# Kernel tuning notes

Hardware: AMD Instinct MI355X
Metric: run time of the kernel (lower is better)

## Reference

```python
import jax, jax.numpy as jnp
import numpy as np

N = 4096
C = 8192
D = 64
MARGIN = 0.1
ALPHA = 32.0


def setup_inputs() -> dict:
    key = jax.random.key(0)
    k1, k2, k3, k4 = jax.random.split(key, 4)
    embeddings = jax.random.normal(k1, (N, D), dtype=jnp.float32)
    labels = jax.random.randint(k2, (N,), 0, C)
    # kaiming_normal_(mode='fan_out') on a (C, D) tensor -> std = sqrt(2/C)
    mean_proxies = jax.random.normal(k3, (C, D), dtype=jnp.float32) * np.sqrt(2.0 / C)
    log_variance_proxies = jax.random.normal(k4, (C, D), dtype=jnp.float32) * np.sqrt(2.0 / C)
    return {
        "embeddings": embeddings,
        "labels": labels,
        "mean_proxies": mean_proxies,
        "log_variance_proxies": log_variance_proxies,
    }


def _mls_scores(e, mu, logvar):
    """score[i,j] = -0.5 * sum_d[(e_id - mu_jd)^2 * exp(-logvar_jd) + logvar_jd].
    Expanded into GEMMs to avoid materializing the (N, C, D) broadcast tensor."""
    inv_var = jnp.exp(-logvar)                                  # (C, D)
    e2_term = (e * e) @ inv_var.T                               # (N, C)
    cross = e @ (mu * inv_var).T                                # (N, C)
    const = jnp.sum(mu * mu * inv_var + logvar, axis=1)         # (C,)
    return -0.5 * (e2_term - 2.0 * cross + const[None, :])      # (N, C)


def reference(embeddings, labels, mean_proxies, log_variance_proxies):
    score_mat = _mls_scores(embeddings, mean_proxies, log_variance_proxies)  # (N, C)
    pos_mask = jax.nn.one_hot(labels, C, dtype=score_mat.dtype)              # (N, C)

    pos_e = -ALPHA * (score_mat - MARGIN)
    neg_e = ALPHA * (score_mat + MARGIN)
    m = jnp.max(pos_e)  # NOTE: original code uses max(pos_exp) for BOTH terms
    pos_exp = jnp.exp(pos_e - m)
    neg_exp = jnp.exp(neg_e - m)

    counts = jnp.sum(pos_mask, axis=0)                   # (C,)
    num_valid = jnp.sum(counts != 0).astype(score_mat.dtype)

    pos_sim_sum = jnp.sum(jnp.where(pos_mask == 1, pos_exp, 0.0), axis=0)  # (C,)
    neg_sim_sum = jnp.sum(jnp.where(pos_mask == 0, neg_exp, 0.0), axis=0)  # (C,)

    pos_term = jnp.sum(jnp.log1p(pos_sim_sum) + m) / num_valid
    neg_term = jnp.sum(jnp.log1p(neg_sim_sum) + m) / C
    return pos_term + neg_term
```

## Files before the change

kernel.cpp:

```cpp
#include <hip/hip_runtime.h>
#include <hip/hip_bf16.h>
#include <math.h>


#define N_EMB 4096
#define C_CLS 8192
#define D_DIM 64
#define K_DIM 128

typedef __attribute__((ext_vector_type(8))) __bf16 bf16x8;
typedef __attribute__((ext_vector_type(16))) float f32x16;
typedef __attribute__((ext_vector_type(4))) int i32x4;

__device__ __forceinline__ void async_ld16(void* lds, const void* g) {
  __builtin_amdgcn_global_load_lds(
      (__attribute__((address_space(1))) void*)g,
      (__attribute__((address_space(3))) void*)lds, 16, 0, 0);
}

__global__ void k_prep(const float* __restrict__ emb,
                       const float* __restrict__ mp,
                       const float* __restrict__ lvp,
                       __bf16* __restrict__ wsA,
                       __bf16* __restrict__ wsB,
                       float* __restrict__ constv) {
  int wave = (int)((blockIdx.x * blockDim.x + threadIdx.x) >> 6);
  int lane = threadIdx.x & 63;
  if (wave < N_EMB) {
    float e = emb[wave * D_DIM + lane];
    wsA[wave * K_DIM + lane]         = (__bf16)(e * e);
    wsA[wave * K_DIM + D_DIM + lane] = (__bf16)e;
  } else {
    int j = wave - N_EMB;
    float mu = mp[j * D_DIM + lane];
    float lv = lvp[j * D_DIM + lane];
    float iv = __expf(-lv);
    wsB[j * K_DIM + lane]         = (__bf16)iv;
    wsB[j * K_DIM + D_DIM + lane] = (__bf16)(-2.0f * mu * iv);
    float t = fmaf(mu * mu, iv, lv);
    #pragma unroll
    for (int s = 32; s >= 1; s >>= 1) t += __shfl_xor(t, s);
    if (lane == 0) constv[j] = t;
  }
}

__global__ __launch_bounds__(256, 2) void k_main(
    const __bf16* __restrict__ wsA, const __bf16* __restrict__ wsB,
    const float* __restrict__ constv, const int* __restrict__ labels,
    float* __restrict__ wsM, float* __restrict__ wsP, float* __restrict__ wsN) {
  __shared__ __align__(16) char As[32768];
  __shared__ __align__(16) char Bs[32768];

  const int tid = threadIdx.x;
  const int rb = blockIdx.x & 31;
  const int cb = blockIdx.x >> 5;

  const char* Ag = (const char*)(wsA + (size_t)rb * 128 * K_DIM);
  const char* Bg = (const char*)(wsB + (size_t)cb * 128 * K_DIM);
  #pragma unroll
  for (int it = 0; it < 8; ++it) {
    int L = it * 256 + tid;
    int r = L >> 4, cs = L & 15;
    int goff = r * 256 + ((cs ^ (r & 15)) << 4);
    async_ld16(As + L * 16, Ag + goff);
  }
  #pragma unroll
  for (int it = 0; it < 8; ++it) {
    int L = it * 256 + tid;
    int r = L >> 4, cs = L & 15;
    int goff = r * 256 + ((cs ^ (r & 15)) << 4);
    async_ld16(Bs + L * 16, Bg + goff);
  }
  __syncthreads();

  const int wv = tid >> 6, lane = tid & 63;
  const int wr = wv >> 1, wc = wv & 1;
  const int l31 = lane & 31, kg = lane >> 5;
  const int l15 = lane & 15;

  f32x16 acc[2][2];
  #pragma unroll
  for (int mi = 0; mi < 2; ++mi)
    #pragma unroll
    for (int ni = 0; ni < 2; ++ni)
      #pragma unroll
      for (int r = 0; r < 16; ++r) acc[mi][ni][r] = 0.f;

  #pragma unroll
  for (int kk = 0; kk < 8; ++kk) {
    const int c = kk * 2 + kg;
    const int cofs = (c ^ l15) << 4;
    bf16x8 af[2], bfr[2];
    #pragma unroll
    for (int mi = 0; mi < 2; ++mi)
      af[mi] = *(const bf16x8*)(As + (wr * 64 + mi * 32 + l31) * 256 + cofs);
    #pragma unroll
    for (int ni = 0; ni < 2; ++ni)
      bfr[ni] = *(const bf16x8*)(Bs + (wc * 64 + ni * 32 + l31) * 256 + cofs);
    #pragma unroll
    for (int mi = 0; mi < 2; ++mi)
      #pragma unroll
      for (int ni = 0; ni < 2; ++ni)
        acc[mi][ni] = __builtin_amdgcn_mfma_f32_32x32x16_bf16(
            af[mi], bfr[ni], acc[mi][ni], 0, 0, 0);
  }

  __syncthreads();
  float* colred = (float*)As;
  int* labels_s = (int*)(As + 3072);
  float* pc_s   = (float*)(As + 3584);
  if (tid < 128) {
    labels_s[tid] = labels[rb * 128 + tid];
    pc_s[tid] = fmaf(16.0f, constv[cb * 128 + tid], 3.2f);
  }
  __syncthreads();

  i32x4 labv[2][4];
  #pragma unroll
  for (int mi = 0; mi < 2; ++mi)
    #pragma unroll
    for (int g = 0; g < 4; ++g)
      labv[mi][g] = *(const i32x4*)&labels_s[wr * 64 + mi * 32 + 4 * kg + 8 * g];

  #pragma unroll
  for (int ni = 0; ni < 2; ++ni) {
    const int col_local = wc * 64 + ni * 32 + l31;
    const int gcol = cb * 128 + col_local;
    const float pcv = pc_s[col_local];
    float lmax = -1e30f;
    #pragma unroll
    for (int mi = 0; mi < 2; ++mi)
      #pragma unroll
      for (int r = 0; r < 16; ++r)
        lmax = fmaxf(lmax, fmaf(16.0f, acc[mi][ni][r], pcv));
    lmax = fmaxf(lmax, __shfl_xor(lmax, 32));
    float ps = 0.f, ns = 0.f;
    #pragma unroll
    for (int mi = 0; mi < 2; ++mi)
      #pragma unroll
      for (int r = 0; r < 16; ++r) {
        float pe = fmaf(16.0f, acc[mi][ni][r], pcv);
        bool match = (labv[mi][r >> 2][r & 3] == gcol);
        float v = match ? pe : (6.4f - pe);
        float ex = __expf(v - lmax);
        ps += match ? ex : 0.f;
        ns += match ? 0.f : ex;
      }
    ps += __shfl_xor(ps, 32);
    ns += __shfl_xor(ns, 32);
    if (kg == 0) {
      float* cr = &colred[(wr * 128 + col_local) * 3];
      cr[0] = lmax; cr[1] = ps; cr[2] = ns;
    }
  }
  __syncthreads();
  if (tid < 128) {
    const float* c0 = &colred[(0 * 128 + tid) * 3];
    const float* c1 = &colred[(1 * 128 + tid) * 3];
    float M = fmaxf(c0[0], c1[0]);
    float s0 = __expf(c0[0] - M), s1 = __expf(c1[0] - M);
    int gcol = cb * 128 + tid;
    wsM[rb * C_CLS + gcol] = M;
    wsP[rb * C_CLS + gcol] = fmaf(c0[1], s0, c1[1] * s1);
    wsN[rb * C_CLS + gcol] = fmaf(c0[2], s0, c1[2] * s1);
  }
}

__global__ __launch_bounds__(256) void k_red1(
    const float* __restrict__ wsM, const float* __restrict__ wsP,
    const float* __restrict__ wsN, float* __restrict__ Mcol,
    float* __restrict__ Pcol, float* __restrict__ Ncol) {
  __shared__ float red[4][64][3];
  const int tid = threadIdx.x;
  const int col = tid & 63, part = tid >> 6;
  const int j = blockIdx.x * 64 + col;

  float m8[8];
  float M = -1e30f;
  #pragma unroll
  for (int r = 0; r < 8; ++r) {
    m8[r] = wsM[(part * 8 + r) * C_CLS + j];
    M = fmaxf(M, m8[r]);
  }
  float ps = 0.f, ns = 0.f;
  #pragma unroll
  for (int r = 0; r < 8; ++r) {
    float s = __expf(m8[r] - M);
    ps = fmaf(wsP[(part * 8 + r) * C_CLS + j], s, ps);
    ns = fmaf(wsN[(part * 8 + r) * C_CLS + j], s, ns);
  }
  red[part][col][0] = M; red[part][col][1] = ps; red[part][col][2] = ns;
  __syncthreads();
  if (part == 0) {
    float M0 = red[0][col][0], M1 = red[1][col][0];
    float M2 = red[2][col][0], M3 = red[3][col][0];
    float Mx = fmaxf(fmaxf(M0, M1), fmaxf(M2, M3));
    float s0 = __expf(M0 - Mx), s1 = __expf(M1 - Mx);
    float s2 = __expf(M2 - Mx), s3 = __expf(M3 - Mx);
    Mcol[j] = Mx;
    Pcol[j] = fmaf(red[0][col][1], s0, fmaf(red[1][col][1], s1,
              fmaf(red[2][col][1], s2, red[3][col][1] * s3)));
    Ncol[j] = fmaf(red[0][col][2], s0, fmaf(red[1][col][2], s1,
              fmaf(red[2][col][2], s2, red[3][col][2] * s3)));
  }
}

__global__ __launch_bounds__(1024) void k_fin(
    const float* __restrict__ Mcol, const float* __restrict__ Pcol,
    const float* __restrict__ Ncol, const int* __restrict__ labels,
    float* __restrict__ out) {
  __shared__ unsigned char flag[C_CLS];
  __shared__ float sA[16], sB[16];
  __shared__ int sI[16];
  const int tid = threadIdx.x;
  const int wv = tid >> 6, lane = tid & 63;
  for (int i = tid; i < C_CLS; i += 1024) flag[i] = 0;
  __syncthreads();
  for (int i = tid; i < N_EMB; i += 1024) flag[labels[i]] = 1;
  __syncthreads();
  int nv = 0;
  float gm = -1e30f;
  #pragma unroll
  for (int k = 0; k < C_CLS / 1024; ++k) {
    int i = k * 1024 + tid;
    nv += flag[i];
    gm = fmaxf(gm, Mcol[i]);
  }
  #pragma unroll
  for (int s = 32; s >= 1; s >>= 1) {
    gm = fmaxf(gm, __shfl_xor(gm, s));
    nv += __shfl_xor(nv, s);
  }
  if (lane == 0) { sA[wv] = gm; sI[wv] = nv; }
  __syncthreads();
  if (tid == 0) {
    float mm = -1e30f; int n = 0;
    #pragma unroll
    for (int k = 0; k < 16; ++k) { mm = fmaxf(mm, sA[k]); n += sI[k]; }
    sA[0] = mm; sI[0] = n;
  }
  __syncthreads();
  const float m = sA[0];
  const int num_valid = sI[0];
  __syncthreads();
  float pt = 0.f, nt = 0.f;
  #pragma unroll
  for (int k = 0; k < C_CLS / 1024; ++k) {
    int i = k * 1024 + tid;
    float s = __expf(Mcol[i] - m);
    pt += log1pf(Pcol[i] * s);
    nt += log1pf(Ncol[i] * s);
  }
  #pragma unroll
  for (int s = 32; s >= 1; s >>= 1) {
    pt += __shfl_xor(pt, s);
    nt += __shfl_xor(nt, s);
  }
  if (lane == 0) { sA[wv] = pt; sB[wv] = nt; }
  __syncthreads();
  if (tid == 0) {
    float sp = 0.f, sn = 0.f;
    #pragma unroll
    for (int k = 0; k < 16; ++k) { sp += sA[k]; sn += sB[k]; }
    out[0] = (sp + (float)C_CLS * m) / (float)num_valid
           + (sn + (float)C_CLS * m) / (float)C_CLS;
  }
}

extern "C" void kernel_launch(void* const* d_in, const int* in_sizes, int n_in,
                              void* d_out, int out_size, void* d_ws, size_t ws_size,
                              hipStream_t stream) {
  const float* emb    = (const float*)d_in[0];
  const int*   labels = (const int*)d_in[1];
  const float* mp     = (const float*)d_in[2];
  const float* lvp    = (const float*)d_in[3];
  float* out = (float*)d_out;

  char* ws = (char*)d_ws;
  __bf16* wsA   = (__bf16*)ws;
  __bf16* wsB   = (__bf16*)(ws + (1u << 20));
  float* constv = (float*)(ws + 3u * (1u << 20));
  float* wsM    = (float*)(ws + 3u * (1u << 20) + (1u << 15));
  float* wsP    = wsM + 32 * C_CLS;
  float* wsN    = wsP + 32 * C_CLS;
  float* Mcol   = wsN + 32 * C_CLS;
  float* Pcol   = Mcol + C_CLS;
  float* Ncol   = Pcol + C_CLS;

  hipLaunchKernelGGL(k_prep, dim3((N_EMB + C_CLS) / 4), dim3(256), 0, stream,
                     emb, mp, lvp, wsA, wsB, constv);
  hipLaunchKernelGGL(k_main, dim3((N_EMB / 128) * (C_CLS / 128)), dim3(256), 0, stream,
                     wsA, wsB, constv, labels, wsM, wsP, wsN);
  hipLaunchKernelGGL(k_red1, dim3(128), dim3(256), 0, stream,
                     wsM, wsP, wsN, Mcol, Pcol, Ncol);
  hipLaunchKernelGGL(k_fin, dim3(1), dim3(1024), 0, stream,
                     Mcol, Pcol, Ncol, labels, out);
}
```

Baseline: 102.1 us.

## Loop row tiles inside persistent blocks with double-buffered A loads and drop red1

k_main now launches 256 blocks of 512 threads. Each block keeps one 128-column B tile resident and loops over eight 128-row A tiles, double-buffering them with async LDS loads. The online softmax-style max/sum state is carried in registers across row tiles, so only 4 row-group partials per column are written instead of 32. The k_red1 kernel is removed and its merge folded into k_fin. The intent is to cut launch count, partial-sum traffic and per-block prologue cost, at the price of only 256 blocks for the whole GPU (about one per CU) and less latency hiding.

```diff
diff --git a/kernel.cpp b/kernel.cpp
--- a/kernel.cpp
+++ b/kernel.cpp
@@ -44,188 +44,178 @@
   }
 }
 
-__global__ __launch_bounds__(256, 2) void k_main(
+__global__ __launch_bounds__(512, 1) void k_main(
     const __bf16* __restrict__ wsA, const __bf16* __restrict__ wsB,
     const float* __restrict__ constv, const int* __restrict__ labels,
     float* __restrict__ wsM, float* __restrict__ wsP, float* __restrict__ wsN) {
-  __shared__ __align__(16) char As[32768];
+  __shared__ __align__(16) char As[2][32768];
   __shared__ __align__(16) char Bs[32768];
 
   const int tid = threadIdx.x;
-  const int rb = blockIdx.x & 31;
-  const int cb = blockIdx.x >> 5;
-
-  const char* Ag = (const char*)(wsA + (size_t)rb * 128 * K_DIM);
-  const char* Bg = (const char*)(wsB + (size_t)cb * 128 * K_DIM);
-  #pragma unroll
-  for (int it = 0; it < 8; ++it) {
-    int L = it * 256 + tid;
-    int r = L >> 4, cs = L & 15;
-    int goff = r * 256 + ((cs ^ (r & 15)) << 4);
-    async_ld16(As + L * 16, Ag + goff);
-  }
-  #pragma unroll
-  for (int it = 0; it < 8; ++it) {
-    int L = it * 256 + tid;
+  const int cb = blockIdx.x & 63;
+  const int rg = blockIdx.x >> 6;
+
+  const char* Abase = (const char*)wsA + (size_t)rg * 1024 * 256;
+  const char* Bg    = (const char*)wsB + (size_t)cb * 128 * 256;
+
+  #pragma unroll
+  for (int it = 0; it < 4; ++it) {
+    int L = it * 512 + tid;
     int r = L >> 4, cs = L & 15;
     int goff = r * 256 + ((cs ^ (r & 15)) << 4);
     async_ld16(Bs + L * 16, Bg + goff);
   }
-  __syncthreads();
+  #pragma unroll
+  for (int it = 0; it < 4; ++it) {
+    int L = it * 512 + tid;
+    int r = L >> 4, cs = L & 15;
+    int goff = r * 256 + ((cs ^ (r & 15)) << 4);
+    async_ld16(As[0] + L * 16, Abase + goff);
+  }
 
   const int wv = tid >> 6, lane = tid & 63;
-  const int wr = wv >> 1, wc = wv & 1;
+  const int wc = wv & 1, wr = wv >> 1;
   const int l31 = lane & 31, kg = lane >> 5;
   const int l15 = lane & 15;
 
-  f32x16 acc[2][2];
-  #pragma unroll
-  for (int mi = 0; mi < 2; ++mi)
+  float pcv[2];
+  #pragma unroll
+  for (int ni = 0; ni < 2; ++ni)
+    pcv[ni] = fmaf(16.0f, constv[cb * 128 + wc * 64 + ni * 32 + l31], 3.2f);
+
+  float rM[2] = {-1e30f, -1e30f}, rP[2] = {0.f, 0.f}, rN[2] = {0.f, 0.f};
+
+  __syncthreads();
+
+  for (int t = 0; t < 8; ++t) {
+    if (t < 7) {
+      const char* Agn = Abase + (size_t)(t + 1) * 32768;
+      #pragma unroll
+      for (int it = 0; it < 4; ++it) {
+        int L = it * 512 + tid;
+        int r = L >> 4, cs = L & 15;
+        int goff = r * 256 + ((cs ^ (r & 15)) << 4);
+        async_ld16(As[(t + 1) & 1] + L * 16, Agn + goff);
+      }
+    }
+    const char* Ac = As[t & 1];
+
+    f32x16 acc[2];
     #pragma unroll
     for (int ni = 0; ni < 2; ++ni)
       #pragma unroll
-      for (int r = 0; r < 16; ++r) acc[mi][ni][r] = 0.f;
-
-  #pragma unroll
-  for (int kk = 0; kk < 8; ++kk) {
-    const int c = kk * 2 + kg;
-    const int cofs = (c ^ l15) << 4;
-    bf16x8 af[2], bfr[2];
-    #pragma unroll
-    for (int mi = 0; mi < 2; ++mi)
-      af[mi] = *(const bf16x8*)(As + (wr * 64 + mi * 32 + l31) * 256 + cofs);
-    #pragma unroll
-    for (int ni = 0; ni < 2; ++ni)
-      bfr[ni] = *(const bf16x8*)(Bs + (wc * 64 + ni * 32 + l31) * 256 + cofs);
-    #pragma unroll
-    for (int mi = 0; mi < 2; ++mi)
-      #pragma unroll
-      for (int ni = 0; ni < 2; ++ni)
-        acc[mi][ni] = __builtin_amdgcn_mfma_f32_32x32x16_bf16(
-            af[mi], bfr[ni], acc[mi][ni], 0, 0, 0);
-  }
-
-  __syncthreads();
-  float* colred = (float*)As;
-  int* labels_s = (int*)(As + 3072);
-  float* pc_s   = (float*)(As + 3584);
-  if (tid < 128) {
-    labels_s[tid] = labels[rb * 128 + tid];
-    pc_s[tid] = fmaf(16.0f, constv[cb * 128 + tid], 3.2f);
-  }
-  __syncthreads();
-
-  i32x4 labv[2][4];
-  #pragma unroll
-  for (int mi = 0; mi < 2; ++mi)
+      for (int r = 0; r < 16; ++r) acc[ni][r] = 0.f;
+
+    #pragma unroll
+    for (int kk = 0; kk < 8; ++kk) {
+      const int c = kk * 2 + kg;
+      const int cofs = (c ^ l15) << 4;
+      bf16x8 af = *(const bf16x8*)(Ac + (wr * 32 + l31) * 256 + cofs);
+      bf16x8 b0 = *(const bf16x8*)(Bs + (wc * 64 + l31) * 256 + cofs);
+      bf16x8 b1 = *(const bf16x8*)(Bs + (wc * 64 + 32 + l31) * 256 + cofs);
+      acc[0] = __builtin_amdgcn_mfma_f32_32x32x16_bf16(af, b0, acc[0], 0, 0, 0);
+      acc[1] = __builtin_amdgcn_mfma_f32_32x32x16_bf16(af, b1, acc[1], 0, 0, 0);
+    }
+
+    const int rowbase = rg * 1024 + t * 128 + wr * 32 + 4 * kg;
+    i32x4 labv[4];
     #pragma unroll
     for (int g = 0; g < 4; ++g)
-      labv[mi][g] = *(const i32x4*)&labels_s[wr * 64 + mi * 32 + 4 * kg + 8 * g];
-
-  #pragma unroll
-  for (int ni = 0; ni < 2; ++ni) {
-    const int col_local = wc * 64 + ni * 32 + l31;
-    const int gcol = cb * 128 + col_local;
-    const float pcv = pc_s[col_local];
-    float lmax = -1e30f;
-    #pragma unroll
-    for (int mi = 0; mi < 2; ++mi)
+      labv[g] = *(const i32x4*)&labels[rowbase + 8 * g];
+
+    #pragma unroll
+    for (int ni = 0; ni < 2; ++ni) {
+      const int gcol = cb * 128 + wc * 64 + ni * 32 + l31;
+      float lmax = -1e30f;
       #pragma unroll
       for (int r = 0; r < 16; ++r)
-        lmax = fmaxf(lmax, fmaf(16.0f, acc[mi][ni][r], pcv));
-    lmax = fmaxf(lmax, __shfl_xor(lmax, 32));
-    float ps = 0.f, ns = 0.f;
-    #pragma unroll
-    for (int mi = 0; mi < 2; ++mi)
+        lmax = fmaxf(lmax, fmaf(16.0f, acc[ni][r], pcv[ni]));
+      lmax = fmaxf(lmax, __shfl_xor(lmax, 32));
+      float ps = 0.f, ns = 0.f;
       #pragma unroll
       for (int r = 0; r < 16; ++r) {
-        float pe = fmaf(16.0f, acc[mi][ni][r], pcv);
-        bool match = (labv[mi][r >> 2][r & 3] == gcol);
+        float pe = fmaf(16.0f, acc[ni][r], pcv[ni]);
+        bool match = (labv[r >> 2][r & 3] == gcol);
         float v = match ? pe : (6.4f - pe);
         float ex = __expf(v - lmax);
         ps += match ? ex : 0.f;
         ns += match ? 0.f : ex;
       }
-    ps += __shfl_xor(ps, 32);
-    ns += __shfl_xor(ns, 32);
-    if (kg == 0) {
-      float* cr = &colred[(wr * 128 + col_local) * 3];
-      cr[0] = lmax; cr[1] = ps; cr[2] = ns;
+      ps += __shfl_xor(ps, 32);
+      ns += __shfl_xor(ns, 32);
+      float nM = fmaxf(rM[ni], lmax);
+      float sO = __expf(rM[ni] - nM), sN = __expf(lmax - nM);
+      rP[ni] = fmaf(rP[ni], sO, ps * sN);
+      rN[ni] = fmaf(rN[ni], sO, ns * sN);
+      rM[ni] = nM;
+    }
+    __syncthreads();
+  }
+
+  float* colred = (float*)As[0];
+  if (kg == 0) {
+    #pragma unroll
+    for (int ni = 0; ni < 2; ++ni) {
+      int cl = wc * 64 + ni * 32 + l31;
+      float* cr = &colred[(wr * 128 + cl) * 3];
+      cr[0] = rM[ni]; cr[1] = rP[ni]; cr[2] = rN[ni];
     }
   }
   __syncthreads();
   if (tid < 128) {
-    const float* c0 = &colred[(0 * 128 + tid) * 3];
-    const float* c1 = &colred[(1 * 128 + tid) * 3];
-    float M = fmaxf(c0[0], c1[0]);
-    float s0 = __expf(c0[0] - M), s1 = __expf(c1[0] - M);
+    float M = -1e30f;
+    #pragma unroll
+    for (int w = 0; w < 4; ++w) M = fmaxf(M, colred[(w * 128 + tid) * 3]);
+    float P = 0.f, Nn = 0.f;
+    #pragma unroll
+    for (int w = 0; w < 4; ++w) {
+      const float* cr = &colred[(w * 128 + tid) * 3];
+      float s = __expf(cr[0] - M);
+      P = fmaf(cr[1], s, P);
+      Nn = fmaf(cr[2], s, Nn);
+    }
     int gcol = cb * 128 + tid;
-    wsM[rb * C_CLS + gcol] = M;
-    wsP[rb * C_CLS + gcol] = fmaf(c0[1], s0, c1[1] * s1);
-    wsN[rb * C_CLS + gcol] = fmaf(c0[2], s0, c1[2] * s1);
-  }
-}
-
-__global__ __launch_bounds__(256) void k_red1(
+    wsM[rg * C_CLS + gcol] = M;
+    wsP[rg * C_CLS + gcol] = P;
+    wsN[rg * C_CLS + gcol] = Nn;
+  }
+}
+
+__global__ __launch_bounds__(1024) void k_fin(
     const float* __restrict__ wsM, const float* __restrict__ wsP,
-    const float* __restrict__ wsN, float* __restrict__ Mcol,
-    float* __restrict__ Pcol, float* __restrict__ Ncol) {
-  __shared__ float red[4][64][3];
-  const int tid = threadIdx.x;
-  const int col = tid & 63, part = tid >> 6;
-  const int j = blockIdx.x * 64 + col;
-
-  float m8[8];
-  float M = -1e30f;
-  #pragma unroll
-  for (int r = 0; r < 8; ++r) {
-    m8[r] = wsM[(part * 8 + r) * C_CLS + j];
-    M = fmaxf(M, m8[r]);
-  }
-  float ps = 0.f, ns = 0.f;
-  #pragma unroll
-  for (int r = 0; r < 8; ++r) {
-    float s = __expf(m8[r] - M);
-    ps = fmaf(wsP[(part * 8 + r) * C_CLS + j], s, ps);
-    ns = fmaf(wsN[(part * 8 + r) * C_CLS + j], s, ns);
-  }
-  red[part][col][0] = M; red[part][col][1] = ps; red[part][col][2] = ns;
-  __syncthreads();
-  if (part == 0) {
-    float M0 = red[0][col][0], M1 = red[1][col][0];
-    float M2 = red[2][col][0], M3 = red[3][col][0];
-    float Mx = fmaxf(fmaxf(M0, M1), fmaxf(M2, M3));
-    float s0 = __expf(M0 - Mx), s1 = __expf(M1 - Mx);
-    float s2 = __expf(M2 - Mx), s3 = __expf(M3 - Mx);
-    Mcol[j] = Mx;
-    Pcol[j] = fmaf(red[0][col][1], s0, fmaf(red[1][col][1], s1,
-              fmaf(red[2][col][1], s2, red[3][col][1] * s3)));
-    Ncol[j] = fmaf(red[0][col][2], s0, fmaf(red[1][col][2], s1,
-              fmaf(red[2][col][2], s2, red[3][col][2] * s3)));
-  }
-}
-
-__global__ __launch_bounds__(1024) void k_fin(
-    const float* __restrict__ Mcol, const float* __restrict__ Pcol,
-    const float* __restrict__ Ncol, const int* __restrict__ labels,
+    const float* __restrict__ wsN, const int* __restrict__ labels,
     float* __restrict__ out) {
   __shared__ unsigned char flag[C_CLS];
   __shared__ float sA[16], sB[16];
   __shared__ int sI[16];
   const int tid = threadIdx.x;
   const int wv = tid >> 6, lane = tid & 63;
+
+  float colM[8], colP[8], colN[8];
+  float gm = -1e30f;
+  #pragma unroll
+  for (int k = 0; k < 8; ++k) {
+    int j = k * 1024 + tid;
+    float m0 = wsM[0 * C_CLS + j], m1 = wsM[1 * C_CLS + j];
+    float m2 = wsM[2 * C_CLS + j], m3 = wsM[3 * C_CLS + j];
+    float M = fmaxf(fmaxf(m0, m1), fmaxf(m2, m3));
+    float s0 = __expf(m0 - M), s1 = __expf(m1 - M);
+    float s2 = __expf(m2 - M), s3 = __expf(m3 - M);
+    colM[k] = M;
+    colP[k] = fmaf(wsP[0 * C_CLS + j], s0, fmaf(wsP[1 * C_CLS + j], s1,
+              fmaf(wsP[2 * C_CLS + j], s2, wsP[3 * C_CLS + j] * s3)));
+    colN[k] = fmaf(wsN[0 * C_CLS + j], s0, fmaf(wsN[1 * C_CLS + j], s1,
+              fmaf(wsN[2 * C_CLS + j], s2, wsN[3 * C_CLS + j] * s3)));
+    gm = fmaxf(gm, M);
+  }
+
   for (int i = tid; i < C_CLS; i += 1024) flag[i] = 0;
   __syncthreads();
   for (int i = tid; i < N_EMB; i += 1024) flag[labels[i]] = 1;
   __syncthreads();
   int nv = 0;
-  float gm = -1e30f;
-  #pragma unroll
-  for (int k = 0; k < C_CLS / 1024; ++k) {
-    int i = k * 1024 + tid;
-    nv += flag[i];
-    gm = fmaxf(gm, Mcol[i]);
-  }
+  #pragma unroll
+  for (int k = 0; k < 8; ++k) nv += flag[k * 1024 + tid];
   #pragma unroll
   for (int s = 32; s >= 1; s >>= 1) {
     gm = fmaxf(gm, __shfl_xor(gm, s));
@@ -245,11 +235,10 @@
   __syncthreads();
   float pt = 0.f, nt = 0.f;
   #pragma unroll
-  for (int k = 0; k < C_CLS / 1024; ++k) {
-    int i = k * 1024 + tid;
-    float s = __expf(Mcol[i] - m);
-    pt += log1pf(Pcol[i] * s);
-    nt += log1pf(Ncol[i] * s);
+  for (int k = 0; k < 8; ++k) {
+    float s = __expf(colM[k] - m);
+    pt += log1pf(colP[k] * s);
+    nt += log1pf(colN[k] * s);
   }
   #pragma unroll
   for (int s = 32; s >= 1; s >>= 1) {
@@ -281,18 +270,13 @@
   __bf16* wsB   = (__bf16*)(ws + (1u << 20));
   float* constv = (float*)(ws + 3u * (1u << 20));
   float* wsM    = (float*)(ws + 3u * (1u << 20) + (1u << 15));
-  float* wsP    = wsM + 32 * C_CLS;
-  float* wsN    = wsP + 32 * C_CLS;
-  float* Mcol   = wsN + 32 * C_CLS;
-  float* Pcol   = Mcol + C_CLS;
-  float* Ncol   = Pcol + C_CLS;
+  float* wsP    = wsM + 4 * C_CLS;
+  float* wsN    = wsP + 4 * C_CLS;
 
   hipLaunchKernelGGL(k_prep, dim3((N_EMB + C_CLS) / 4), dim3(256), 0, stream,
                      emb, mp, lvp, wsA, wsB, constv);
-  hipLaunchKernelGGL(k_main, dim3((N_EMB / 128) * (C_CLS / 128)), dim3(256), 0, stream,
+  hipLaunchKernelGGL(k_main, dim3(4 * (C_CLS / 128)), dim3(512), 0, stream,
                      wsA, wsB, constv, labels, wsM, wsP, wsN);
-  hipLaunchKernelGGL(k_red1, dim3(128), dim3(256), 0, stream,
-                     wsM, wsP, wsN, Mcol, Pcol, Ncol);
   hipLaunchKernelGGL(k_fin, dim3(1), dim3(1024), 0, stream,
-                     Mcol, Pcol, Ncol, labels, out);
-}
+                     wsM, wsP, wsN, labels, out);
+}
```

Result: no change. 104.1 us (+1.9%).

## Fuse bf16 operand preparation into main GEMM kernel, drop prep launch

Applied to the files above, without the earlier changes.

Removes the separate k_prep kernel and its bf16 workspace. Each k_main block now reads fp32 embeddings and proxies directly, computes squares, exp(-logvar), scaled means and per-class constants, and writes swizzled bf16 tiles into LDS. Labels are read from global memory instead of being staged in LDS, which drops one barrier. This saves a launch and the workspace round trip. In exchange every block recomputes its tiles (each proxy tile is redone 32 times, each embedding tile 64 times) and reads twice as many bytes of fp32 input.

```diff
diff --git a/kernel.cpp b/kernel.cpp
--- a/kernel.cpp
+++ b/kernel.cpp
@@ -12,64 +12,61 @@
 typedef __attribute__((ext_vector_type(16))) float f32x16;
 typedef __attribute__((ext_vector_type(4))) int i32x4;
 
-__device__ __forceinline__ void async_ld16(void* lds, const void* g) {
-  __builtin_amdgcn_global_load_lds(
-      (__attribute__((address_space(1))) void*)g,
-      (__attribute__((address_space(3))) void*)lds, 16, 0, 0);
-}
-
-__global__ void k_prep(const float* __restrict__ emb,
-                       const float* __restrict__ mp,
-                       const float* __restrict__ lvp,
-                       __bf16* __restrict__ wsA,
-                       __bf16* __restrict__ wsB,
-                       float* __restrict__ constv) {
-  int wave = (int)((blockIdx.x * blockDim.x + threadIdx.x) >> 6);
-  int lane = threadIdx.x & 63;
-  if (wave < N_EMB) {
-    float e = emb[wave * D_DIM + lane];
-    wsA[wave * K_DIM + lane]         = (__bf16)(e * e);
-    wsA[wave * K_DIM + D_DIM + lane] = (__bf16)e;
-  } else {
-    int j = wave - N_EMB;
-    float mu = mp[j * D_DIM + lane];
-    float lv = lvp[j * D_DIM + lane];
-    float iv = __expf(-lv);
-    wsB[j * K_DIM + lane]         = (__bf16)iv;
-    wsB[j * K_DIM + D_DIM + lane] = (__bf16)(-2.0f * mu * iv);
-    float t = fmaf(mu * mu, iv, lv);
-    #pragma unroll
-    for (int s = 32; s >= 1; s >>= 1) t += __shfl_xor(t, s);
-    if (lane == 0) constv[j] = t;
-  }
-}
-
 __global__ __launch_bounds__(256, 2) void k_main(
-    const __bf16* __restrict__ wsA, const __bf16* __restrict__ wsB,
-    const float* __restrict__ constv, const int* __restrict__ labels,
+    const float* __restrict__ emb, const float* __restrict__ mp,
+    const float* __restrict__ lvp, const int* __restrict__ labels,
     float* __restrict__ wsM, float* __restrict__ wsP, float* __restrict__ wsN) {
   __shared__ __align__(16) char As[32768];
   __shared__ __align__(16) char Bs[32768];
+  __shared__ float pc_s[128];
 
   const int tid = threadIdx.x;
   const int rb = blockIdx.x & 31;
   const int cb = blockIdx.x >> 5;
 
-  const char* Ag = (const char*)(wsA + (size_t)rb * 128 * K_DIM);
-  const char* Bg = (const char*)(wsB + (size_t)cb * 128 * K_DIM);
-  #pragma unroll
-  for (int it = 0; it < 8; ++it) {
-    int L = it * 256 + tid;
-    int r = L >> 4, cs = L & 15;
-    int goff = r * 256 + ((cs ^ (r & 15)) << 4);
-    async_ld16(As + L * 16, Ag + goff);
-  }
-  #pragma unroll
-  for (int it = 0; it < 8; ++it) {
-    int L = it * 256 + tid;
-    int r = L >> 4, cs = L & 15;
-    int goff = r * 256 + ((cs ^ (r & 15)) << 4);
-    async_ld16(Bs + L * 16, Bg + goff);
+  #pragma unroll
+  for (int i = 0; i < 4; ++i) {
+    int q = i * 256 + tid;
+    int r = q >> 3, dc = q & 7;
+    const float* src = emb + (size_t)(rb * 128 + r) * D_DIM + dc * 8;
+    float4 a = *(const float4*)src;
+    float4 b = *(const float4*)(src + 4);
+    bf16x8 sq = {(__bf16)(a.x*a.x), (__bf16)(a.y*a.y), (__bf16)(a.z*a.z),
+                 (__bf16)(a.w*a.w), (__bf16)(b.x*b.x), (__bf16)(b.y*b.y),
+                 (__bf16)(b.z*b.z), (__bf16)(b.w*b.w)};
+    bf16x8 ev = {(__bf16)a.x, (__bf16)a.y, (__bf16)a.z, (__bf16)a.w,
+                 (__bf16)b.x, (__bf16)b.y, (__bf16)b.z, (__bf16)b.w};
+    int s1 = dc ^ (r & 15);
+    *(bf16x8*)(As + r * 256 + s1 * 16) = sq;
+    *(bf16x8*)(As + r * 256 + (s1 ^ 8) * 16) = ev;
+  }
+  #pragma unroll
+  for (int i = 0; i < 4; ++i) {
+    int q = i * 256 + tid;
+    int c = q >> 3, dc = q & 7;
+    const float* mus = mp + (size_t)(cb * 128 + c) * D_DIM + dc * 8;
+    const float* lvs = lvp + (size_t)(cb * 128 + c) * D_DIM + dc * 8;
+    float4 m0 = *(const float4*)mus, m1 = *(const float4*)(mus + 4);
+    float4 l0 = *(const float4*)lvs, l1 = *(const float4*)(lvs + 4);
+    float iv0 = __expf(-l0.x), iv1 = __expf(-l0.y);
+    float iv2 = __expf(-l0.z), iv3 = __expf(-l0.w);
+    float iv4 = __expf(-l1.x), iv5 = __expf(-l1.y);
+    float iv6 = __expf(-l1.z), iv7 = __expf(-l1.w);
+    bf16x8 ivv = {(__bf16)iv0, (__bf16)iv1, (__bf16)iv2, (__bf16)iv3,
+                  (__bf16)iv4, (__bf16)iv5, (__bf16)iv6, (__bf16)iv7};
+    bf16x8 mv = {(__bf16)(-2.0f*m0.x*iv0), (__bf16)(-2.0f*m0.y*iv1),
+                 (__bf16)(-2.0f*m0.z*iv2), (__bf16)(-2.0f*m0.w*iv3),
+                 (__bf16)(-2.0f*m1.x*iv4), (__bf16)(-2.0f*m1.y*iv5),
+                 (__bf16)(-2.0f*m1.z*iv6), (__bf16)(-2.0f*m1.w*iv7)};
+    int s1 = dc ^ (c & 15);
+    *(bf16x8*)(Bs + c * 256 + s1 * 16) = ivv;
+    *(bf16x8*)(Bs + c * 256 + (s1 ^ 8) * 16) = mv;
+    float t = fmaf(m0.x*m0.x, iv0, l0.x) + fmaf(m0.y*m0.y, iv1, l0.y)
+            + fmaf(m0.z*m0.z, iv2, l0.z) + fmaf(m0.w*m0.w, iv3, l0.w)
+            + fmaf(m1.x*m1.x, iv4, l1.x) + fmaf(m1.y*m1.y, iv5, l1.y)
+            + fmaf(m1.z*m1.z, iv6, l1.z) + fmaf(m1.w*m1.w, iv7, l1.w);
+    t += __shfl_xor(t, 1); t += __shfl_xor(t, 2); t += __shfl_xor(t, 4);
+    if (dc == 0) pc_s[c] = fmaf(16.0f, t, 3.2f);
   }
   __syncthreads();
 
@@ -107,20 +104,13 @@
 
   __syncthreads();
   float* colred = (float*)As;
-  int* labels_s = (int*)(As + 3072);
-  float* pc_s   = (float*)(As + 3584);
-  if (tid < 128) {
-    labels_s[tid] = labels[rb * 128 + tid];
-    pc_s[tid] = fmaf(16.0f, constv[cb * 128 + tid], 3.2f);
-  }
-  __syncthreads();
 
   i32x4 labv[2][4];
   #pragma unroll
   for (int mi = 0; mi < 2; ++mi)
     #pragma unroll
     for (int g = 0; g < 4; ++g)
-      labv[mi][g] = *(const i32x4*)&labels_s[wr * 64 + mi * 32 + 4 * kg + 8 * g];
+      labv[mi][g] = *(const i32x4*)&labels[rb * 128 + wr * 64 + mi * 32 + 4 * kg + 8 * g];
 
   #pragma unroll
   for (int ni = 0; ni < 2; ++ni) {
@@ -277,20 +267,15 @@
   float* out = (float*)d_out;
 
   char* ws = (char*)d_ws;
-  __bf16* wsA   = (__bf16*)ws;
-  __bf16* wsB   = (__bf16*)(ws + (1u << 20));
-  float* constv = (float*)(ws + 3u * (1u << 20));
-  float* wsM    = (float*)(ws + 3u * (1u << 20) + (1u << 15));
-  float* wsP    = wsM + 32 * C_CLS;
-  float* wsN    = wsP + 32 * C_CLS;
-  float* Mcol   = wsN + 32 * C_CLS;
-  float* Pcol   = Mcol + C_CLS;
-  float* Ncol   = Pcol + C_CLS;
-
-  hipLaunchKernelGGL(k_prep, dim3((N_EMB + C_CLS) / 4), dim3(256), 0, stream,
-                     emb, mp, lvp, wsA, wsB, constv);
+  float* wsM  = (float*)ws;
+  float* wsP  = wsM + 32 * C_CLS;
+  float* wsN  = wsP + 32 * C_CLS;
+  float* Mcol = wsN + 32 * C_CLS;
+  float* Pcol = Mcol + C_CLS;
+  float* Ncol = Pcol + C_CLS;
+
   hipLaunchKernelGGL(k_main, dim3((N_EMB / 128) * (C_CLS / 128)), dim3(256), 0, stream,
-                     wsA, wsB, constv, labels, wsM, wsP, wsN);
+                     emb, mp, lvp, labels, wsM, wsP, wsN);
   hipLaunchKernelGGL(k_red1, dim3(128), dim3(256), 0, stream,
                      wsM, wsP, wsN, Mcol, Pcol, Ncol);
   hipLaunchKernelGGL(k_fin, dim3(1), dim3(1024), 0, stream,
```

After: 104.1 us. Within noise of the previous version (+1.9%).
